# Kernel tuning notes

Measured on AMD Instinct MI355X. Metric: run time of the kernel, lower is better.

## Reference

```python
import jax, jax.numpy as jnp
import numpy as np

B, N, DIN, DH, DOUT, H = 64, 512, 256, 512, 256, 4


def setup_inputs() -> dict:
    key = jax.random.key(0)
    ks = jax.random.split(key, 11)
    s = 0.02
    return {
        "x": jax.random.normal(ks[0], (B, N, DIN), jnp.float32),
        # block 0 (in=DIN): per-head embed Linear(DIN,DH) and KQ Linear(DIN,2*DH)
        "e_w0": jax.random.normal(ks[1], (H, DIN, DH), jnp.float32) * s,
        "e_b0": jax.random.normal(ks[2], (H, DH), jnp.float32) * s,
        "kq_w0": jax.random.normal(ks[3], (H, DIN, 2 * DH), jnp.float32) * s,
        "kq_b0": jax.random.normal(ks[4], (H, 2 * DH), jnp.float32) * s,
        # block 1 (in=DH)
        "e_w1": jax.random.normal(ks[5], (H, DH, DH), jnp.float32) * s,
        "e_b1": jax.random.normal(ks[6], (H, DH), jnp.float32) * s,
        "kq_w1": jax.random.normal(ks[7], (H, DH, 2 * DH), jnp.float32) * s,
        "kq_b1": jax.random.normal(ks[8], (H, 2 * DH), jnp.float32) * s,
        # output projection Linear(DH, DOUT)
        "proj_w": jax.random.normal(ks[9], (DH, DOUT), jnp.float32) * s,
        "proj_b": jax.random.normal(ks[10], (DOUT,), jnp.float32) * s,
    }


def _multi_attn(x, ew, eb, kqw, kqb):
    # x: [b,n,d]; ew: [h,d,e]; kqw: [h,d,2e]. num_hidden_layers=2 => each MLP is one Linear.
    embs = jnp.einsum('bnd,hde->hbne', x, ew) + eb[:, None, None, :]
    kq = jnp.einsum('bnd,hdf->hbnf', x, kqw) + kqb[:, None, None, :]
    K, Q = jnp.split(kq, 2, axis=-1)  # torch.chunk order: K first, then Q
    A = jax.nn.softmax(jnp.einsum('hbqe,hbke->hbqk', Q, K), axis=-1)  # unscaled
    out = jnp.einsum('hbqk,hbke->hbqe', A, embs)
    return out.mean(axis=0)  # mean over heads


def reference(x, e_w0, e_b0, kq_w0, kq_b0, e_w1, e_b1, kq_w1, kq_b1, proj_w, proj_b):
    h = _multi_attn(x, e_w0, e_b0, kq_w0, kq_b0)
    h = _multi_attn(h, e_w1, e_b1, kq_w1, kq_b1)
    return h @ proj_w + proj_b
```

## Files before the change

### kernel.cpp

```cpp
#include <hip/hip_runtime.h>

typedef _Float16 half8 __attribute__((ext_vector_type(8)));
typedef _Float16 half4 __attribute__((ext_vector_type(4)));
typedef float floatx4 __attribute__((ext_vector_type(4)));

#define B_    64
#define N_    512
#define DIN_  256
#define DH_   512
#define DOUT_ 256
#define H_    4
#define BN_   (B_ * N_)

#define WAIT_VM4_LGKM0() __builtin_amdgcn_s_waitcnt(0x0074)
#define WAIT_VM0_LGKM0() __builtin_amdgcn_s_waitcnt(0x0070)
#define WAIT_VM4()       __builtin_amdgcn_s_waitcnt(0x0F74)
#define WAIT_VM0()       __builtin_amdgcn_s_waitcnt(0x0F70)
#define MEMBAR()         __asm__ __volatile__("" ::: "memory")
#define BAR()            do { MEMBAR(); __builtin_amdgcn_s_barrier(); MEMBAR(); } while (0)

__device__ static inline void async_copy16(const _Float16* g, _Float16* l) {
    __builtin_amdgcn_global_load_lds(
        (const __attribute__((address_space(1))) void*)g,
        (__attribute__((address_space(3))) void*)l, 16, 0, 0);
}

template <bool OUT_F16>
__global__ __launch_bounds__(256)
void gemm_f16(const _Float16* __restrict__ A, long long aS1, long long aS2, int lda, long long aSeg,
              const _Float16* __restrict__ B, long long bS1, long long bS2, int ldb, long long bSeg,
              void* __restrict__ Cv, long long cS1, long long cS2, int ldc,
              int K, const float* __restrict__ bias, int biasMode,
              long long biasS1, long long biasS2, int zShift)
{
    __shared__ __align__(16) _Float16 As[3][128 * 32];
    __shared__ __align__(16) _Float16 Bs[3][128 * 32];

    const int tid  = threadIdx.x;
    const int wave = tid >> 6;
    const int lane = tid & 63;
    const int quad = lane >> 4;
    const int r16  = lane & 15;

    const int z  = blockIdx.z;
    const int z1 = z >> zShift;
    const int z2 = z & ((1 << zShift) - 1);

    const int gx = gridDim.x, gy = gridDim.y;
    const int T = gx * gy;
    int lin = blockIdx.y * gx + blockIdx.x;
    int id2 = (T & 7) ? lin : ((lin & 7) * (T >> 3) + (lin >> 3));
    const int m0 = (id2 / gx) * 128;
    const int n0 = (id2 % gx) * 128;

    const int srow = lane >> 2;
    const int scol = (((lane & 3) ^ ((lane >> 3) & 3))) * 8;

    const _Float16* gaRow = A + z1 * aS1 + z2 * aS2
                              + (long long)(m0 + wave * 32 + srow) * lda + scol;
    const _Float16* gbRow = B + z1 * bS1 + z2 * bS2
                              + (long long)(n0 + wave * 32 + srow) * ldb + scol;

    const int wm = (wave >> 1) * 64;
    const int wn = (wave & 1) * 64;
    const int gl = (quad ^ ((r16 >> 1) & 3)) * 8;

    floatx4 acc[4][4];
#pragma unroll
    for (int i = 0; i < 4; i++)
#pragma unroll
        for (int j = 0; j < 4; j++) acc[i][j] = (floatx4){0.f, 0.f, 0.f, 0.f};

    auto stage = [&](int p, int k0) {
        const _Float16* a = gaRow + (long long)(k0 >> 9) * aSeg + (k0 & 511);
        const _Float16* b = gbRow + (long long)(k0 >> 9) * bSeg + (k0 & 511);
        _Float16* la = &As[p][wave * 1024];
        _Float16* lb = &Bs[p][wave * 1024];
        async_copy16(a,                    la);
        async_copy16(a + (size_t)16 * lda, la + 512);
        async_copy16(b,                    lb);
        async_copy16(b + (size_t)16 * ldb, lb + 512);
    };

    auto compute = [&](int p) {
        half8 af[4], bf[4];
#pragma unroll
        for (int i = 0; i < 4; i++)
            af[i] = *(const half8*)&As[p][(wm + i * 16 + r16) * 32 + gl];
#pragma unroll
        for (int j = 0; j < 4; j++)
            bf[j] = *(const half8*)&Bs[p][(wn + j * 16 + r16) * 32 + gl];
#pragma unroll
        for (int i = 0; i < 4; i++)
#pragma unroll
            for (int j = 0; j < 4; j++)
                acc[i][j] = __builtin_amdgcn_mfma_f32_16x16x32_f16(
                    bf[j], af[i], acc[i][j], 0, 0, 0);
    };

    const int niter = K >> 5;
    stage(0, 0);
    stage(1, 32);
    int pNext = 2;
    int pCur  = 0;
    for (int it = 0; it < niter - 1; ++it) {
        MEMBAR(); WAIT_VM4_LGKM0();
        __builtin_amdgcn_s_barrier();
        MEMBAR();
        if (it + 2 < niter) stage(pNext, (it + 2) << 5);
        compute(pCur);
        MEMBAR();
        pNext = (pNext == 2) ? 0 : pNext + 1;
        pCur  = (pCur  == 2) ? 0 : pCur  + 1;
    }
    MEMBAR(); WAIT_VM0_LGKM0();
    __builtin_amdgcn_s_barrier(); MEMBAR();
    compute(pCur);

    const float* bz = bias + z1 * biasS1 + z2 * biasS2;
    float*    Cf = (float*)Cv    + z1 * cS1 + z2 * cS2;
    _Float16* Ch = (_Float16*)Cv + z1 * cS1 + z2 * cS2;
#pragma unroll
    for (int i = 0; i < 4; i++) {
        const int row = m0 + wm + i * 16 + r16;
#pragma unroll
        for (int j = 0; j < 4; j++) {
            const int col = n0 + wn + j * 16 + quad * 4;
            float v0 = acc[i][j][0], v1 = acc[i][j][1],
                  v2 = acc[i][j][2], v3 = acc[i][j][3];
            if (biasMode == 1) {
                v0 += bz[col]; v1 += bz[col + 1];
                v2 += bz[col + 2]; v3 += bz[col + 3];
            } else if (biasMode == 2) {
                const float bv = bz[row];
                v0 += bv; v1 += bv; v2 += bv; v3 += bv;
            }
            const size_t idx = (size_t)row * ldc + col;
            if (OUT_F16) {
                half4 hv = {(_Float16)v0, (_Float16)v1, (_Float16)v2, (_Float16)v3};
                *(half4*)&Ch[idx] = hv;
            } else {
                float4 fv = {v0, v1, v2, v3};
                *(float4*)&Cf[idx] = fv;
            }
        }
    }
}

template <bool OUT_F16>
__global__ __launch_bounds__(512, 2)
void gemm256(const _Float16* __restrict__ A, long long aS1, long long aS2, int lda, long long aSeg, int aSh,
             const _Float16* __restrict__ B, long long bS1, long long bS2, int ldb, long long bSeg, int bSh,
             void* __restrict__ Cv, long long cS1, long long cS2, int ldc,
             int K, const float* __restrict__ bias, int biasMode,
             long long biasS1, long long biasS2, int zShift, int zLoop, int zOrd)
{
    extern __shared__ __align__(16) _Float16 lds[];
    _Float16* AsB = lds;
    _Float16* BsB = lds + 2 * 256 * 64;

    const int tid  = threadIdx.x;
    const int wave = tid >> 6;
    const int lane = tid & 63;
    const int quad = lane >> 4;
    const int r16  = lane & 15;
    const int wr   = wave >> 2;
    const int wc   = wave & 3;

    const int pz = blockIdx.z;
    int zz0, zz1;
    if (zOrd == 1) {
        const int b = (pz & 7) | ((pz >> 5) << 3);
        const int h = (pz >> 3) & 3;
        zz0 = (b << 2) + h; zz1 = zz0;
    } else if (zOrd == 2) {
        const int b = pz & 15;
        const int h = pz >> 4;
        zz0 = (b << 2) + h; zz1 = zz0 + 64;
    } else {
        zz0 = pz * zLoop; zz1 = zz0 + (zLoop - 1);
    }
    const int zMask = (1 << zShift) - 1;

    const int aTSh = aSh - 6, aTMk = (1 << aTSh) - 1;
    const int bTSh = bSh - 6, bTMk = (1 << bTSh) - 1;

    const int ntiles = K >> 6;
    const int ntSh   = __builtin_ctz(ntiles);
    const int ntHMsk = (ntiles >> 1) - 1;
    const int TTh    = (ntiles * zLoop) >> 1;

    const int gx = gridDim.x, gy = gridDim.y;
    const int T_ = gx * gy;
    int lin = blockIdx.y * gx + blockIdx.x;
    int id2 = (T_ & 7) ? lin : ((lin & 7) * (T_ >> 3) + (lin >> 3));
    const int m0 = (id2 / gx) * 256;
    const int n0 = (id2 % gx) * 256;

    const int sr  = tid >> 3;
    const int swz = ((tid & 7) ^ (sr & 7)) * 8;

    const _Float16* gaA0 = A + (long long)(zz0 >> zShift) * aS1 + (long long)(zz0 & zMask) * aS2
                             + (long long)(m0 + sr) * lda + swz;
    const _Float16* gaA1 = A + (long long)(zz1 >> zShift) * aS1 + (long long)(zz1 & zMask) * aS2
                             + (long long)(m0 + sr) * lda + swz;
    const _Float16* gbB0 = B + (long long)(zz0 >> zShift) * bS1 + (long long)(zz0 & zMask) * bS2
                             + (long long)(n0 + sr) * ldb + swz;
    const _Float16* gbB1 = B + (long long)(zz1 >> zShift) * bS1 + (long long)(zz1 & zMask) * bS2
                             + (long long)(n0 + sr) * ldb + swz;

    const int arow = wr * 64 + r16;
    const int brow = wc * 32 + r16;
    const int rsw  = r16 & 7;
    const int gxk0 = (quad ^ rsw) * 8;
    const int gxk1 = ((4 + quad) ^ rsw) * 8;

    floatx4 acc[8][4];
#pragma unroll
    for (int i = 0; i < 8; i++)
#pragma unroll
        for (int j = 0; j < 4; j++) acc[i][j] = (floatx4){0.f, 0.f, 0.f, 0.f};

    half8 af[4][2], bf0s[2][2], bf1s[2][2];

    auto stageA = [&](int buf, int h, int T) {
        const int tz = T >> ntSh, tk = T & (ntiles - 1);
        const _Float16* s = (tz ? gaA1 : gaA0) + (long long)(h * 128) * lda
                          + (long long)(tk >> aTSh) * aSeg + ((tk & aTMk) << 6);
        _Float16* d = AsB + buf * 16384 + h * 8192 + wave * 512;
        async_copy16(s, d);
        async_copy16(s + (long long)64 * lda, d + 4096);
    };
    auto stageB = [&](int buf, int h, int T) {
        const int tz = T >> ntSh, tk = T & (ntiles - 1);
        const _Float16* s = (tz ? gbB1 : gbB0) + (long long)(h * 128) * ldb
                          + (long long)(tk >> bTSh) * bSeg + ((tk & bTMk) << 6);
        _Float16* d = BsB + buf * 16384 + h * 8192 + wave * 512;
        async_copy16(s, d);
        async_copy16(s + (long long)64 * ldb, d + 4096);
    };

    auto epi = [&](int zz) {
        const int z1 = zz >> zShift, z2 = zz & zMask;
        const float* bz = bias + (long long)z1 * biasS1 + (long long)z2 * biasS2;
        float*    Cf = (float*)Cv    + (long long)z1 * cS1 + (long long)z2 * cS2;
        _Float16* Ch = (_Float16*)Cv + (long long)z1 * cS1 + (long long)z2 * cS2;
#pragma unroll
        for (int f = 0; f < 8; f++) {
            const int row = m0 + (f >> 2) * 128 + wr * 64 + (f & 3) * 16 + r16;
#pragma unroll
            for (int j = 0; j < 4; j++) {
                const int col = n0 + (j >> 1) * 128 + wc * 32 + (j & 1) * 16 + quad * 4;
                float v0 = acc[f][j][0], v1 = acc[f][j][1],
                      v2 = acc[f][j][2], v3 = acc[f][j][3];
                if (biasMode == 1) {
                    v0 += bz[col]; v1 += bz[col + 1];
                    v2 += bz[col + 2]; v3 += bz[col + 3];
                } else if (biasMode == 2) {
                    const float bv = bz[row];
                    v0 += bv; v1 += bv; v2 += bv; v3 += bv;
                }
                const size_t idx = (size_t)row * ldc + col;
                if (OUT_F16) {
                    half4 hv = {(_Float16)v0, (_Float16)v1, (_Float16)v2, (_Float16)v3};
                    *(half4*)&Ch[idx] = hv;
                } else {
                    float4 fv = {v0, v1, v2, v3};
                    *(float4*)&Cf[idx] = fv;
                }
            }
        }
    };

#define LOAD_AF(RH, BUF) do { \
    const _Float16* ab_ = AsB + (BUF) * 16384 + ((RH) * 128 + arow) * 64; \
    _Pragma("unroll") \
    for (int i5 = 0; i5 < 4; i5++) { \
        af[i5][0] = *(const half8*)(ab_ + i5 * 1024 + gxk0); \
        af[i5][1] = *(const half8*)(ab_ + i5 * 1024 + gxk1); \
    } \
} while (0)

#define LOAD_BF(DST, CH, BUF) do { \
    const _Float16* bb_ = BsB + (BUF) * 16384 + ((CH) * 128 + brow) * 64; \
    _Pragma("unroll") \
    for (int j5 = 0; j5 < 2; j5++) { \
        DST[j5][0] = *(const half8*)(bb_ + j5 * 1024 + gxk0); \
        DST[j5][1] = *(const half8*)(bb_ + j5 * 1024 + gxk1); \
    } \
} while (0)

#define MFMA16(RH, CH, BFS) do { \
    _Pragma("unroll") \
    for (int i6 = 0; i6 < 4; i6++) { \
        _Pragma("unroll") \
        for (int j6 = 0; j6 < 2; j6++) { \
            floatx4 c_ = acc[(RH) * 4 + i6][(CH) * 2 + j6]; \
            c_ = __builtin_amdgcn_mfma_f32_16x16x32_f16(BFS[j6][0], af[i6][0], c_, 0, 0, 0); \
            c_ = __builtin_amdgcn_mfma_f32_16x16x32_f16(BFS[j6][1], af[i6][1], c_, 0, 0, 0); \
            acc[(RH) * 4 + i6][(CH) * 2 + j6] = c_; \
        } \
    } \
} while (0)

    stageA(0, 0, 0);
    stageB(0, 1, 0);
    stageA(0, 1, 0);
    stageB(0, 0, 0);
    stageA(1, 0, 1);
    stageB(1, 1, 1);
    WAIT_VM4();
    BAR();

    int zi = 0;
    for (int it = 0; it < TTh; ++it) {
        const int T = it * 2;
        const bool full = (it < TTh - 1);

        LOAD_AF(0, 0); LOAD_BF(bf0s, 0, 0);
        stageA(1, 1, T + 1);
        BAR();
        __builtin_amdgcn_s_setprio(1); MFMA16(0, 0, bf0s); __builtin_amdgcn_s_setprio(0);
        BAR();
        LOAD_BF(bf1s, 1, 0);
        stageB(1, 0, T + 1);
        BAR();
        __builtin_amdgcn_s_setprio(1); MFMA16(0, 1, bf1s); __builtin_amdgcn_s_setprio(0);
        BAR();
        LOAD_AF(1, 0);
        if (full) stageA(0, 0, T + 2);
        BAR();
        __builtin_amdgcn_s_setprio(1); MFMA16(1, 1, bf1s); __builtin_amdgcn_s_setprio(0);
        BAR();
        if (full) stageB(0, 1, T + 2);
        BAR();
        __builtin_amdgcn_s_setprio(1); MFMA16(1, 0, bf0s); __builtin_amdgcn_s_setprio(0);
        if (full) WAIT_VM4(); else WAIT_VM0();
        BAR();
        LOAD_AF(0, 1); LOAD_BF(bf0s, 0, 1);
        if (full) stageA(0, 1, T + 2);
        BAR();
        __builtin_amdgcn_s_setprio(1); MFMA16(0, 0, bf0s); __builtin_amdgcn_s_setprio(0);
        BAR();
        LOAD_BF(bf1s, 1, 1);
        if (full) stageB(0, 0, T + 2);
        BAR();
        __builtin_amdgcn_s_setprio(1); MFMA16(0, 1, bf1s); __builtin_amdgcn_s_setprio(0);
        BAR();
        LOAD_AF(1, 1);
        if (full) stageA(1, 0, T + 3);
        BAR();
        __builtin_amdgcn_s_setprio(1); MFMA16(1, 1, bf1s); __builtin_amdgcn_s_setprio(0);
        BAR();
        if (full) stageB(1, 1, T + 3);
        BAR();
        __builtin_amdgcn_s_setprio(1); MFMA16(1, 0, bf0s); __builtin_amdgcn_s_setprio(0);
        if (full) WAIT_VM4();
        BAR();

        if (((it + 1) & ntHMsk) == 0) {
            epi(zi ? zz1 : zz0);
            ++zi;
#pragma unroll
            for (int i7 = 0; i7 < 8; i7++)
#pragma unroll
                for (int j7 = 0; j7 < 4; j7++)
                    acc[i7][j7] = (floatx4){0.f, 0.f, 0.f, 0.f};
        }
    }

#undef LOAD_AF
#undef LOAD_BF
#undef MFMA16
}

__global__ __launch_bounds__(256)
void softmax_f16(_Float16* __restrict__ S)
{
    const int row  = blockIdx.x * 4 + (threadIdx.x >> 6);
    const int lane = threadIdx.x & 63;
    _Float16* s = S + (size_t)row * 512 + lane * 8;
    half8 h = *(const half8*)s;
    float v[8];
    float mx = -1e30f;
#pragma unroll
    for (int j = 0; j < 8; j++) { v[j] = (float)h[j]; mx = fmaxf(mx, v[j]); }
#pragma unroll
    for (int off = 32; off; off >>= 1) mx = fmaxf(mx, __shfl_xor(mx, off));
    float sum = 0.f;
#pragma unroll
    for (int j = 0; j < 8; j++) { v[j] = __expf(v[j] - mx); sum += v[j]; }
#pragma unroll
    for (int off = 32; off; off >>= 1) sum += __shfl_xor(sum, off);
    const float inv = 0.25f / sum;
#pragma unroll
    for (int j = 0; j < 8; j++) h[j] = (_Float16)(v[j] * inv);
    *(half8*)s = h;
}

__global__ __launch_bounds__(256)
void cvt_multi(const float* __restrict__ s0, _Float16* __restrict__ d0, int c0,
               const float* __restrict__ s1, _Float16* __restrict__ d1, int c1,
               const float* __restrict__ s2, _Float16* __restrict__ d2, int c2,
               const float* __restrict__ s3, _Float16* __restrict__ d3, int c3)
{
    int i = blockIdx.x * 256 + threadIdx.x;
    const float* s; _Float16* d;
    if (i < c0) { s = s0; d = d0; }
    else { i -= c0;
        if (i < c1) { s = s1; d = d1; }
        else { i -= c1;
            if (i < c2) { s = s2; d = d2; }
            else { i -= c2; s = s3; d = d3; } } }
    const float4 f = ((const float4*)s)[i];
    half4 hv = {(_Float16)f.x, (_Float16)f.y, (_Float16)f.z, (_Float16)f.w};
    *(half4*)(d + (size_t)i * 4) = hv;
}

__global__ __launch_bounds__(256)
void transpose_cvt(const float* __restrict__ in, _Float16* __restrict__ out,
                   int R, int C)
{
    __shared__ float tile[32][33];
    const int g  = blockIdx.z;
    const int c0 = blockIdx.x * 32;
    const int r0 = blockIdx.y * 32;
    const float* inp  = in  + (size_t)g * R * C;
    _Float16*    outp = out + (size_t)g * R * C;
#pragma unroll
    for (int i = threadIdx.y; i < 32; i += 8)
        tile[i][threadIdx.x] = inp[(size_t)(r0 + i) * C + c0 + threadIdx.x];
    __syncthreads();
#pragma unroll
    for (int i = threadIdx.y; i < 32; i += 8)
        outp[(size_t)(c0 + i) * R + r0 + threadIdx.x] = (_Float16)tile[threadIdx.x][i];
}

__global__ __launch_bounds__(256)
void small_ops(const float* __restrict__ kq_w0, const float* __restrict__ kq_b0,
               const float* __restrict__ kq_w1, const float* __restrict__ kq_b1,
               const _Float16* __restrict__ projwT, const float* __restrict__ e_b1,
               const float* __restrict__ e_b0,
               float* __restrict__ w0, float* __restrict__ w1,
               float* __restrict__ be1p, float* __restrict__ sb0)
{
    const int blk = blockIdx.x;
    if (blk < 4) {
        const int t = blk * 256 + threadIdx.x;
        const int h = t >> 8, d = t & 255;
        const float* wk = kq_w0 + ((size_t)(h << 8) + d) * (2 * DH_);
        const float* bq = kq_b0 + (size_t)h * 2 * DH_ + DH_;
        float s = 0.f;
        for (int e = 0; e < DH_; e++) s += wk[e] * bq[e];
        w0[t] = s;
    } else if (blk < 12) {
        const int t = (blk - 4) * 256 + threadIdx.x;
        const int h = t >> 9, d = t & 511;
        const float* wk = kq_w1 + ((size_t)(h << 9) + d) * (2 * DH_);
        const float* bq = kq_b1 + (size_t)h * 2 * DH_ + DH_;
        float s = 0.f;
        for (int e = 0; e < DH_; e++) s += wk[e] * bq[e];
        w1[t] = s;
    } else if (blk < 16) {
        const int t = (blk - 12) * 256 + threadIdx.x;
        const int h = t >> 8, o = t & 255;
        const _Float16* pw = projwT + (size_t)o * DH_;
        const float*    eb = e_b1 + (size_t)h * DH_;
        float s = 0.f;
        for (int d = 0; d < DH_; d++) s += (float)pw[d] * eb[d];
        be1p[t] = s;
    } else {
        const int e = (blk - 16) * 256 + threadIdx.x;
        sb0[e] = 0.25f * (e_b0[e] + e_b0[DH_ + e] + e_b0[2 * DH_ + e] + e_b0[3 * DH_ + e]);
    }
}

__global__ __launch_bounds__(256)
void compute_v(const _Float16* __restrict__ x, const float* __restrict__ w,
               float* __restrict__ V, int Kin)
{
    const int row  = blockIdx.x * 4 + (threadIdx.x >> 6);
    const int lane = threadIdx.x & 63;
    const int b = row >> 9, n = row & 511;
    const _Float16* xr = x + (size_t)row * Kin;
    float s0 = 0.f, s1 = 0.f, s2 = 0.f, s3 = 0.f;
    const int iters = Kin >> 8;
    for (int j = 0; j < iters; j++) {
        const int e = j * 256 + lane * 4;
        const half4  xv = *(const half4*)(xr + e);
        const float4 a0 = *(const float4*)(w + e);
        const float4 a1 = *(const float4*)(w + Kin + e);
        const float4 a2 = *(const float4*)(w + 2 * Kin + e);
        const float4 a3 = *(const float4*)(w + 3 * Kin + e);
        const float x0 = (float)xv[0], x1 = (float)xv[1],
                    x2 = (float)xv[2], x3 = (float)xv[3];
        s0 += x0 * a0.x + x1 * a0.y + x2 * a0.z + x3 * a0.w;
        s1 += x0 * a1.x + x1 * a1.y + x2 * a1.z + x3 * a1.w;
        s2 += x0 * a2.x + x1 * a2.y + x2 * a2.z + x3 * a2.w;
        s3 += x0 * a3.x + x1 * a3.y + x2 * a3.z + x3 * a3.w;
    }
#pragma unroll
    for (int off = 32; off; off >>= 1) {
        s0 += __shfl_xor(s0, off); s1 += __shfl_xor(s1, off);
        s2 += __shfl_xor(s2, off); s3 += __shfl_xor(s3, off);
    }
    if (lane == 0) {
        float* vb = V + ((size_t)b * H_) * N_ + n;
        vb[0] = s0; vb[N_] = s1; vb[2 * N_] = s2; vb[3 * N_] = s3;
    }
}

extern "C" void kernel_launch(void* const* d_in, const int* in_sizes, int n_in,
                              void* d_out, int out_size, void* d_ws, size_t ws_size,
                              hipStream_t stream)
{
    (void)in_sizes; (void)n_in; (void)out_size;

    static bool attr_set = false;
    if (!attr_set) {
        hipFuncSetAttribute((const void*)gemm256<true>,
                            hipFuncAttributeMaxDynamicSharedMemorySize, 131072);
        hipFuncSetAttribute((const void*)gemm256<false>,
                            hipFuncAttributeMaxDynamicSharedMemorySize, 131072);
        attr_set = true;
    }

    const float* x      = (const float*)d_in[0];
    const float* e_w0   = (const float*)d_in[1];
    const float* e_b0   = (const float*)d_in[2];
    const float* kq_w0  = (const float*)d_in[3];
    const float* kq_b0  = (const float*)d_in[4];
    const float* e_w1   = (const float*)d_in[5];
    const float* e_b1   = (const float*)d_in[6];
    const float* kq_w1  = (const float*)d_in[7];
    const float* kq_b1  = (const float*)d_in[8];
    const float* proj_w = (const float*)d_in[9];
    const float* proj_b = (const float*)d_in[10];
    float* out = (float*)d_out;

    char* ws = (char*)d_ws;
    size_t off = 0;
    auto alloc = [&](size_t bytes) -> char* {
        char* p = ws + off;
        off += (bytes + 255) & ~(size_t)255;
        return p;
    };

    _Float16* x16    = (_Float16*)alloc((size_t)BN_ * DIN_ * 2);
    _Float16* h1_16  = (_Float16*)alloc((size_t)BN_ * DH_ * 2);
    _Float16* ewT0   = (_Float16*)alloc((size_t)H_ * DH_ * DIN_ * 2);
    _Float16* projwT = (_Float16*)alloc((size_t)DOUT_ * DH_ * 2);
    _Float16* Mt0    = (_Float16*)alloc((size_t)H_ * DIN_ * DIN_ * 2);
    _Float16* Mt1    = (_Float16*)alloc((size_t)H_ * DH_ * DH_ * 2);
    _Float16* We1pT  = (_Float16*)alloc((size_t)H_ * DOUT_ * DH_ * 2);
    float*    be1p   = (float*)alloc((size_t)H_ * DOUT_ * 4);
    float*    w0     = (float*)alloc((size_t)H_ * DIN_ * 4);
    float*    w1     = (float*)alloc((size_t)H_ * DH_ * 4);
    float*    sb0    = (float*)alloc((size_t)DH_ * 4);
    float*    Vb     = (float*)alloc((size_t)B_ * H_ * N_ * 4);
    _Float16* xT     = (_Float16*)alloc((size_t)BN_ * DIN_ * 2);

    const size_t persistAll = off;
    const long long SB = (long long)N_ * N_;
    const size_t SC_FULL  = (size_t)B_ * H_ * N_ * N_ * 2;
    const size_t SC_CHUNK = SC_FULL / 2;
    const size_t A2_SZ    = (size_t)BN_ * H_ * DIN_ * 2;
    const size_t SLACK    = 1u << 20;

    const bool tierA = ws_size >= persistAll + SC_FULL + A2_SZ + SLACK;

    _Float16* Sc = (_Float16*)alloc(tierA ? SC_FULL : SC_CHUNK);
    _Float16* A2 = (_Float16*)alloc(A2_SZ);

    _Float16* kq0_16 = A2;
    _Float16* kq1_16 = kq0_16 + (size_t)H_ * DIN_ * 2 * DH_;
    _Float16* ew1_16 = kq1_16 + (size_t)H_ * DH_ * 2 * DH_;

    auto gemm = [&](bool outF16,
                    const _Float16* A, long long aS1, long long aS2, int lda, long long aSeg,
                    const _Float16* Bp, long long bS1, long long bS2, int ldb, long long bSeg,
                    void* C, long long cS1, long long cS2, int ldc,
                    int M, int Nn, int K, int batches, int zShift,
                    const float* bias, int biasMode, long long biasS1, long long biasS2,
                    int aSh, int bSh, int zLoop, int zOrd) {
        const bool can256 = (M % 256 == 0) && (Nn % 256 == 0) && (K % 128 == 0);
        const bool can128 = (M % 128 == 0) && (Nn % 128 == 0) && (K % 32 == 0)
                          && (aSh == 9) && (bSh == 9) && (zLoop == 1) && (zOrd == 0);
        const long long wg256 = can256
            ? (long long)(M >> 8) * (Nn >> 8) * (batches / zLoop) : 0;
        bool use256;
        if (!can128)            use256 = true;
        else if (!can256)       use256 = false;
        else                    use256 = (wg256 >= 192) || (wg256 >= 32 && wg256 * 4 < 128);
        if (use256) {
            dim3 grid(Nn / 256, M / 256, batches / zLoop), block(512);
            if (outF16)
                gemm256<true><<<grid, block, 131072, stream>>>(A, aS1, aS2, lda, aSeg, aSh,
                    Bp, bS1, bS2, ldb, bSeg, bSh, C, cS1, cS2, ldc, K, bias, biasMode, biasS1, biasS2, zShift, zLoop, zOrd);
            else
                gemm256<false><<<grid, block, 131072, stream>>>(A, aS1, aS2, lda, aSeg, aSh,
                    Bp, bS1, bS2, ldb, bSeg, bSh, C, cS1, cS2, ldc, K, bias, biasMode, biasS1, biasS2, zShift, zLoop, zOrd);
        } else {
            dim3 grid(Nn / 128, M / 128, batches), block(256);
            if (outF16)
                gemm_f16<true><<<grid, block, 0, stream>>>(A, aS1, aS2, lda, aSeg,
                    Bp, bS1, bS2, ldb, bSeg, C, cS1, cS2, ldc, K, bias, biasMode, biasS1, biasS2, zShift);
            else
                gemm_f16<false><<<grid, block, 0, stream>>>(A, aS1, aS2, lda, aSeg,
                    Bp, bS1, bS2, ldb, bSeg, C, cS1, cS2, ldc, K, bias, biasMode, biasS1, biasS2, zShift);
        }
    };

    {
        const int c0 = BN_ * DIN_ / 4;
        const int c1 = H_ * DIN_ * 2 * DH_ / 4;
        const int c2 = H_ * DH_ * 2 * DH_ / 4;
        const int c3 = H_ * DH_ * DH_ / 4;
        cvt_multi<<<(c0 + c1 + c2 + c3) / 256, 256, 0, stream>>>(
            x, x16, c0, kq_w0, kq0_16, c1, kq_w1, kq1_16, c2, e_w1, ew1_16, c3);
    }
    transpose_cvt<<<dim3(DH_ / 32, DIN_ / 32, H_), dim3(32, 8), 0, stream>>>(e_w0, ewT0, DIN_, DH_);
    transpose_cvt<<<dim3(DOUT_ / 32, DH_ / 32, 1), dim3(32, 8), 0, stream>>>(proj_w, projwT, DH_, DOUT_);
    transpose_cvt<<<dim3(DIN_ / 32, N_ / 32, B_), dim3(32, 8), 0, stream>>>(x, xT, N_, DIN_);
    small_ops<<<18, 256, 0, stream>>>(kq_w0, kq_b0, kq_w1, kq_b1,
                                      projwT, e_b1, e_b0, w0, w1, be1p, sb0);

    gemm(true, kq0_16, 0, (long long)DIN_ * 2 * DH_, 2 * DH_, 512,
         kq0_16 + DH_, 0, (long long)DIN_ * 2 * DH_, 2 * DH_, 512,
         Mt0, 0, (long long)DIN_ * DIN_, DIN_,
         DIN_, DIN_, DH_, H_, 2, nullptr, 0, 0, 0, 9, 9, 1, 0);
    gemm(true, kq1_16, 0, (long long)DH_ * 2 * DH_, 2 * DH_, 512,
         kq1_16 + DH_, 0, (long long)DH_ * 2 * DH_, 2 * DH_, 512,
         Mt1, 0, (long long)DH_ * DH_, DH_,
         DH_, DH_, DH_, H_, 2, nullptr, 0, 0, 0, 9, 9, 1, 0);
    gemm(true, projwT, 0, 0, DH_, 512,
         ew1_16, 0, (long long)DH_ * DH_, DH_, 512,
         We1pT, 0, (long long)DOUT_ * DH_, DH_,
         DOUT_, DH_, DH_, H_, 2, nullptr, 0, 0, 0, 9, 9, 1, 0);

    {
        const int CH0  = tierA ? B_ : 32;
        const int NCH0 = B_ / CH0;
        const int sOrd  = tierA ? 1 : 2;
        const int sLoop = tierA ? 1 : 2;
        const size_t GCH = (size_t)CH0 * N_ * H_ * DIN_;
        compute_v<<<BN_ / 4, 256, 0, stream>>>(x16, w0, Vb, DIN_);

        gemm(true, x16, (long long)N_ * DIN_, 0, DIN_, 512,
             Mt0, 0, 0, DIN_, 512,
             A2, (long long)N_ * H_ * DIN_, 0, H_ * DIN_,
             N_, H_ * DIN_, DIN_, B_, 0, nullptr, 0, 0, 0, 9, 9, 2, 0);

        for (int c = 0; c < NCH0; c++) {
            const _Float16* xc  = x16 + (size_t)c * CH0 * N_ * DIN_;
            const _Float16* xTc = xT  + (size_t)c * CH0 * DIN_ * N_;
            _Float16* slot = A2 + (size_t)c * GCH;
            gemm(true, slot, (long long)N_ * H_ * DIN_, DIN_, H_ * DIN_, 512,
                 xc, (long long)N_ * DIN_, 0, DIN_, 512,
                 Sc, (long long)H_ * SB, SB, N_,
                 N_, N_, DIN_, CH0 * H_, 2,
                 Vb + (size_t)c * CH0 * H_ * N_, 1, (long long)H_ * N_, N_, 9, 9, sLoop, sOrd);
            softmax_f16<<<CH0 * H_ * N_ / 4, 256, 0, stream>>>(Sc);
            gemm(true, Sc, (long long)H_ * SB, SB, N_, 512,
                 xTc, (long long)DIN_ * N_, 0, N_, 512,
                 slot, (long long)H_ * N_ * DIN_, (long long)N_ * DIN_, DIN_,
                 N_, DIN_, N_, CH0 * H_, 2, nullptr, 0, 0, 0, 9, 9, 1, 1);
        }
        gemm(true, A2, (long long)H_ * N_ * DIN_, 0, DIN_, (long long)N_ * DIN_,
             ewT0, 0, 0, DIN_, (long long)DH_ * DIN_,
             h1_16, (long long)N_ * DH_, 0, DH_,
             N_, DH_, H_ * DIN_, B_, 0, sb0, 1, 0, 0, 8, 8, 1, 0);
    }

    {
        compute_v<<<BN_ / 4, 256, 0, stream>>>(h1_16, w1, Vb, DH_);
        for (int c = 0; c < 2; c++) {
            const _Float16* hc = h1_16 + (size_t)c * 32 * N_ * DH_;
            _Float16* Scp = tierA ? Sc + (size_t)c * 32 * H_ * SB : Sc;
            gemm(true, hc, (long long)256 * DH_, 0, DH_, 512,
                 Mt1, 0, 0, DH_, 512,
                 A2, (long long)256 * H_ * DH_, 0, H_ * DH_,
                 256, H_ * DH_, DH_, 64, 0, nullptr, 0, 0, 0, 9, 9, 2, 0);
            gemm(true, A2, (long long)N_ * H_ * DH_, DH_, H_ * DH_, 512,
                 hc, (long long)N_ * DH_, 0, DH_, 512,
                 Scp, (long long)H_ * SB, SB, N_,
                 N_, N_, DH_, 32 * H_, 2,
                 Vb + (size_t)c * 32 * H_ * N_, 1, (long long)H_ * N_, N_, 9, 9, 2, 2);
            softmax_f16<<<32 * H_ * N_ / 4, 256, 0, stream>>>(Scp);
            if (!tierA) {
                gemm(true, We1pT, 0, 0, DH_, 512,
                     hc, (long long)N_ * DH_, 0, DH_, 512,
                     A2, (long long)H_ * DOUT_ * N_, 0, N_,
                     H_ * DOUT_, N_, DH_, 32, 0, be1p, 2, 0, 0, 9, 9, 1, 0);
                gemm(false, Scp, (long long)H_ * SB, 0, N_, SB,
                     A2, (long long)H_ * DOUT_ * N_, 0, N_, (long long)DOUT_ * N_,
                     out + (size_t)c * 32 * N_ * DOUT_, (long long)N_ * DOUT_, 0, DOUT_,
                     N_, DOUT_, H_ * N_, 32, 0, proj_b, 1, 0, 0, 9, 9, 1, 0);
            }
        }
        if (tierA) {
            gemm(true, We1pT, 0, 0, DH_, 512,
                 h1_16, (long long)N_ * DH_, 0, DH_, 512,
                 A2, (long long)H_ * DOUT_ * N_, 0, N_,
                 H_ * DOUT_, N_, DH_, B_, 0, be1p, 2, 0, 0, 9, 9, 1, 0);
            gemm(false, Sc, (long long)H_ * SB, 0, N_, SB,
                 A2, (long long)H_ * DOUT_ * N_, 0, N_, (long long)DOUT_ * N_,
                 out, (long long)N_ * DOUT_, 0, DOUT_,
                 N_, DOUT_, H_ * N_, B_, 0, proj_b, 1, 0, 0, 9, 9, 1, 0);
        }
    }
}
```

Measured before the change: 895.0 us.

## Fold key-bias term into projection GEMM bias and split-K the final PV GEMM

Drops the separate compute_v kernels by passing the per-head bias vectors (w0, w1) as column biases to the x·Mt GEMMs, so the score GEMMs no longer need a row-bias term. Also adds a split-K mode to gemm_f16 and uses it for the final attention×projected-embedding GEMM in the non-tierA path. Partial results go to scratch and a new combine kernel sums them with proj_b. The aim is to remove two small kernel launches and give the small-grid PV GEMM more blocks. In exchange it adds an extra partial-buffer write/read and another launch, and it only affects the non-tierA path.

```diff
diff --git a/kernel.cpp b/kernel.cpp
--- a/kernel.cpp
+++ b/kernel.cpp
@@ -31,7 +31,8 @@
               const _Float16* __restrict__ B, long long bS1, long long bS2, int ldb, long long bSeg,
               void* __restrict__ Cv, long long cS1, long long cS2, int ldc,
               int K, const float* __restrict__ bias, int biasMode,
-              long long biasS1, long long biasS2, int zShift)
+              long long biasS1, long long biasS2, int zShift,
+              int splitK, long long cSplit)
 {
     __shared__ __align__(16) _Float16 As[3][128 * 32];
     __shared__ __align__(16) _Float16 Bs[3][128 * 32];
@@ -42,9 +43,13 @@
     const int quad = lane >> 4;
     const int r16  = lane & 15;
 
-    const int z  = blockIdx.z;
-    const int z1 = z >> zShift;
-    const int z2 = z & ((1 << zShift) - 1);
+    int zz = blockIdx.z;
+    int half = 0;
+    if (splitK) { half = zz & 1; zz >>= 1; }
+    const int z1 = zz >> zShift;
+    const int z2 = zz & ((1 << zShift) - 1);
+    const int Keff  = splitK ? (K >> 1) : K;
+    const int kBase = splitK ? half * (K >> 1) : 0;
 
     const int gx = gridDim.x, gy = gridDim.y;
     const int T = gx * gy;
@@ -71,7 +76,8 @@
 #pragma unroll
         for (int j = 0; j < 4; j++) acc[i][j] = (floatx4){0.f, 0.f, 0.f, 0.f};
 
-    auto stage = [&](int p, int k0) {
+    auto stage = [&](int p, int k0r) {
+        const int k0 = k0r + kBase;
         const _Float16* a = gaRow + (long long)(k0 >> 9) * aSeg + (k0 & 511);
         const _Float16* b = gbRow + (long long)(k0 >> 9) * bSeg + (k0 & 511);
         _Float16* la = &As[p][wave * 1024];
@@ -98,7 +104,7 @@
                     bf[j], af[i], acc[i][j], 0, 0, 0);
     };
 
-    const int niter = K >> 5;
+    const int niter = Keff >> 5;
     stage(0, 0);
     stage(1, 32);
     int pNext = 2;
@@ -118,8 +124,8 @@
     compute(pCur);
 
     const float* bz = bias + z1 * biasS1 + z2 * biasS2;
-    float*    Cf = (float*)Cv    + z1 * cS1 + z2 * cS2;
-    _Float16* Ch = (_Float16*)Cv + z1 * cS1 + z2 * cS2;
+    float*    Cf = (float*)Cv    + z1 * cS1 + z2 * cS2 + (long long)half * cSplit;
+    _Float16* Ch = (_Float16*)Cv + z1 * cS1 + z2 * cS2 + (long long)half * cSplit;
 #pragma unroll
     for (int i = 0; i < 4; i++) {
         const int row = m0 + wm + i * 16 + r16;
@@ -145,6 +151,19 @@
             }
         }
     }
+}
+
+__global__ __launch_bounds__(256)
+void combine_pv(const float* __restrict__ p, long long partStride,
+                const float* __restrict__ bias, float* __restrict__ out)
+{
+    const size_t i = ((size_t)blockIdx.x * 256 + threadIdx.x) * 4;
+    const float4 a = *(const float4*)(p + i);
+    const float4 b = *(const float4*)(p + partStride + i);
+    const float4 bb = *(const float4*)(bias + (i & (DOUT_ - 1)));
+    float4 r = {a.x + b.x + bb.x, a.y + b.y + bb.y,
+                a.z + b.z + bb.z, a.w + b.w + bb.w};
+    *(float4*)(out + i) = r;
 }
 
 template <bool OUT_F16>
@@ -475,41 +494,6 @@
     }
 }
 
-__global__ __launch_bounds__(256)
-void compute_v(const _Float16* __restrict__ x, const float* __restrict__ w,
-               float* __restrict__ V, int Kin)
-{
-    const int row  = blockIdx.x * 4 + (threadIdx.x >> 6);
-    const int lane = threadIdx.x & 63;
-    const int b = row >> 9, n = row & 511;
-    const _Float16* xr = x + (size_t)row * Kin;
-    float s0 = 0.f, s1 = 0.f, s2 = 0.f, s3 = 0.f;
-    const int iters = Kin >> 8;
-    for (int j = 0; j < iters; j++) {
-        const int e = j * 256 + lane * 4;
-        const half4  xv = *(const half4*)(xr + e);
-        const float4 a0 = *(const float4*)(w + e);
-        const float4 a1 = *(const float4*)(w + Kin + e);
-        const float4 a2 = *(const float4*)(w + 2 * Kin + e);
-        const float4 a3 = *(const float4*)(w + 3 * Kin + e);
-        const float x0 = (float)xv[0], x1 = (float)xv[1],
-                    x2 = (float)xv[2], x3 = (float)xv[3];
-        s0 += x0 * a0.x + x1 * a0.y + x2 * a0.z + x3 * a0.w;
-        s1 += x0 * a1.x + x1 * a1.y + x2 * a1.z + x3 * a1.w;
-        s2 += x0 * a2.x + x1 * a2.y + x2 * a2.z + x3 * a2.w;
-        s3 += x0 * a3.x + x1 * a3.y + x2 * a3.z + x3 * a3.w;
-    }
-#pragma unroll
-    for (int off = 32; off; off >>= 1) {
-        s0 += __shfl_xor(s0, off); s1 += __shfl_xor(s1, off);
-        s2 += __shfl_xor(s2, off); s3 += __shfl_xor(s3, off);
-    }
-    if (lane == 0) {
-        float* vb = V + ((size_t)b * H_) * N_ + n;
-        vb[0] = s0; vb[N_] = s1; vb[2 * N_] = s2; vb[3 * N_] = s3;
-    }
-}
-
 extern "C" void kernel_launch(void* const* d_in, const int* in_sizes, int n_in,
                               void* d_out, int out_size, void* d_ws, size_t ws_size,
                               hipStream_t stream)
@@ -557,7 +541,6 @@
     float*    w0     = (float*)alloc((size_t)H_ * DIN_ * 4);
     float*    w1     = (float*)alloc((size_t)H_ * DH_ * 4);
     float*    sb0    = (float*)alloc((size_t)DH_ * 4);
-    float*    Vb     = (float*)alloc((size_t)B_ * H_ * N_ * 4);
     _Float16* xT     = (_Float16*)alloc((size_t)BN_ * DIN_ * 2);
 
     const size_t persistAll = off;
@@ -604,10 +587,10 @@
             dim3 grid(Nn / 128, M / 128, batches), block(256);
             if (outF16)
                 gemm_f16<true><<<grid, block, 0, stream>>>(A, aS1, aS2, lda, aSeg,
-                    Bp, bS1, bS2, ldb, bSeg, C, cS1, cS2, ldc, K, bias, biasMode, biasS1, biasS2, zShift);
+                    Bp, bS1, bS2, ldb, bSeg, C, cS1, cS2, ldc, K, bias, biasMode, biasS1, biasS2, zShift, 0, 0);
             else
                 gemm_f16<false><<<grid, block, 0, stream>>>(A, aS1, aS2, lda, aSeg,
-                    Bp, bS1, bS2, ldb, bSeg, C, cS1, cS2, ldc, K, bias, biasMode, biasS1, biasS2, zShift);
+                    Bp, bS1, bS2, ldb, bSeg, C, cS1, cS2, ldc, K, bias, biasMode, biasS1, biasS2, zShift, 0, 0);
         }
     };
 
@@ -644,12 +627,11 @@
         const int sOrd  = tierA ? 1 : 2;
         const int sLoop = tierA ? 1 : 2;
         const size_t GCH = (size_t)CH0 * N_ * H_ * DIN_;
-        compute_v<<<BN_ / 4, 256, 0, stream>>>(x16, w0, Vb, DIN_);
 
         gemm(true, x16, (long long)N_ * DIN_, 0, DIN_, 512,
              Mt0, 0, 0, DIN_, 512,
              A2, (long long)N_ * H_ * DIN_, 0, H_ * DIN_,
-             N_, H_ * DIN_, DIN_, B_, 0, nullptr, 0, 0, 0, 9, 9, 2, 0);
+             N_, H_ * DIN_, DIN_, B_, 0, w0, 1, 0, 0, 9, 9, 2, 0);
 
         for (int c = 0; c < NCH0; c++) {
             const _Float16* xc  = x16 + (size_t)c * CH0 * N_ * DIN_;
@@ -659,7 +641,7 @@
                  xc, (long long)N_ * DIN_, 0, DIN_, 512,
                  Sc, (long long)H_ * SB, SB, N_,
                  N_, N_, DIN_, CH0 * H_, 2,
-                 Vb + (size_t)c * CH0 * H_ * N_, 1, (long long)H_ * N_, N_, 9, 9, sLoop, sOrd);
+                 nullptr, 0, 0, 0, 9, 9, sLoop, sOrd);
             softmax_f16<<<CH0 * H_ * N_ / 4, 256, 0, stream>>>(Sc);
             gemm(true, Sc, (long long)H_ * SB, SB, N_, 512,
                  xTc, (long long)DIN_ * N_, 0, N_, 512,
@@ -673,29 +655,36 @@
     }
 
     {
-        compute_v<<<BN_ / 4, 256, 0, stream>>>(h1_16, w1, Vb, DH_);
         for (int c = 0; c < 2; c++) {
             const _Float16* hc = h1_16 + (size_t)c * 32 * N_ * DH_;
             _Float16* Scp = tierA ? Sc + (size_t)c * 32 * H_ * SB : Sc;
             gemm(true, hc, (long long)256 * DH_, 0, DH_, 512,
                  Mt1, 0, 0, DH_, 512,
                  A2, (long long)256 * H_ * DH_, 0, H_ * DH_,
-                 256, H_ * DH_, DH_, 64, 0, nullptr, 0, 0, 0, 9, 9, 2, 0);
+                 256, H_ * DH_, DH_, 64, 0, w1, 1, 0, 0, 9, 9, 2, 0);
             gemm(true, A2, (long long)N_ * H_ * DH_, DH_, H_ * DH_, 512,
                  hc, (long long)N_ * DH_, 0, DH_, 512,
                  Scp, (long long)H_ * SB, SB, N_,
                  N_, N_, DH_, 32 * H_, 2,
-                 Vb + (size_t)c * 32 * H_ * N_, 1, (long long)H_ * N_, N_, 9, 9, 2, 2);
+                 nullptr, 0, 0, 0, 9, 9, 2, 2);
             softmax_f16<<<32 * H_ * N_ / 4, 256, 0, stream>>>(Scp);
             if (!tierA) {
                 gemm(true, We1pT, 0, 0, DH_, 512,
                      hc, (long long)N_ * DH_, 0, DH_, 512,
                      A2, (long long)H_ * DOUT_ * N_, 0, N_,
                      H_ * DOUT_, N_, DH_, 32, 0, be1p, 2, 0, 0, 9, 9, 1, 0);
-                gemm(false, Scp, (long long)H_ * SB, 0, N_, SB,
-                     A2, (long long)H_ * DOUT_ * N_, 0, N_, (long long)DOUT_ * N_,
-                     out + (size_t)c * 32 * N_ * DOUT_, (long long)N_ * DOUT_, 0, DOUT_,
-                     N_, DOUT_, H_ * N_, 32, 0, proj_b, 1, 0, 0, 9, 9, 1, 0);
+                float* pPart = (float*)(A2 + (size_t)32 * H_ * DOUT_ * N_);
+                const long long partStride = (long long)32 * N_ * DOUT_;
+                {
+                    dim3 grid(DOUT_ / 128, N_ / 128, 64), block(256);
+                    gemm_f16<false><<<grid, block, 0, stream>>>(
+                        Scp, (long long)H_ * SB, 0, N_, SB,
+                        A2, (long long)H_ * DOUT_ * N_, 0, N_, (long long)DOUT_ * N_,
+                        pPart, (long long)N_ * DOUT_, 0, DOUT_,
+                        H_ * N_, nullptr, 0, 0, 0, 0, 1, partStride);
+                }
+                combine_pv<<<(unsigned)(partStride / 4 / 256), 256, 0, stream>>>(
+                    pPart, partStride, proj_b, out + (size_t)c * 32 * N_ * DOUT_);
             }
         }
         if (tierA) {
```

Measured after the change: 841.5 us. -6.0%, faster.
